# Kernel tuning notes

Hardware: AMD Instinct MI355X
Metric: run time of the kernel (lower is better)

Reference implementation:

```python
import jax, jax.numpy as jnp
import numpy as np

KH = KW = 2  # kernel_size
SH = SW = 2  # stride (== kernel, non-overlapping)

def setup_inputs() -> dict:
    key = jax.random.key(0)
    x = jax.random.normal(key, (64, 256, 112, 112), dtype=jnp.float32)
    return {"x": x}

def reference(x) -> jnp.ndarray:
    # Eval-mode stochastic pool: out = sum_k w_k * (w_k / sum_j w_j) over each
    # KHxKW window of relu(x); windows with zero sum produce 0.
    t = jax.nn.relu(x)
    B, C, H, W = t.shape
    Ho, Wo = H // SH, W // SW
    # stride == kernel -> non-overlapping windows via reshape (matches unfold)
    w = t.reshape(B, C, Ho, KH, Wo, KW).transpose(0, 1, 2, 4, 3, 5)
    w = w.reshape(B, C, Ho, Wo, KH * KW)
    s = w.sum(axis=-1)                      # [B,C,Ho,Wo]
    s_adj = jnp.where(s == 0, jnp.ones_like(s), s)
    out = (w * w).sum(axis=-1) / s_adj      # sum(w * w/sum(w))
    return out
```

## Files before the change

### kernel.cpp

```cpp
#include <hip/hip_runtime.h>


typedef float v4f __attribute__((ext_vector_type(4)));
typedef float v2f __attribute__((ext_vector_type(2)));

#define NCHUNK 28672u
#define CH_IN  7168u
#define CH_OUT 1792u

__global__ __launch_bounds__(256) void stoch_pool2d_kernel(
    const float* __restrict__ in, float* __restrict__ out) {
    __shared__ float lds[CH_IN];
    const unsigned int t = threadIdx.x;

    for (unsigned int c = blockIdx.x; c < NCHUNK; c += gridDim.x) {
        const v4f* src = reinterpret_cast<const v4f*>(in + (size_t)c * CH_IN);

        v4f r[7];
#pragma unroll
        for (int i = 0; i < 7; ++i)
            r[i] = __builtin_nontemporal_load(src + (i * 256u + t));
#pragma unroll
        for (int i = 0; i < 7; ++i)
            reinterpret_cast<v4f*>(lds)[i * 256u + t] = r[i];
        __syncthreads();

        float* dst = out + (size_t)c * CH_OUT;
        const v2f* l2 = reinterpret_cast<const v2f*>(lds);
#pragma unroll
        for (int i = 0; i < 7; ++i) {
            unsigned int o    = i * 256u + t;
            unsigned int orow = o / 56u;
            unsigned int ocol = o - orow * 56u;
            v2f top = l2[(2u * orow)      * 56u + ocol];
            v2f bot = l2[(2u * orow + 1u) * 56u + ocol];

            float a0 = fmaxf(top.x, 0.f), a1 = fmaxf(top.y, 0.f);
            float b0 = fmaxf(bot.x, 0.f), b1 = fmaxf(bot.y, 0.f);
            float s = (a0 + a1) + (b0 + b1);
            float q = (a0 * a0 + a1 * a1) + (b0 * b0 + b1 * b1);
            float v = (s > 0.f) ? q * __builtin_amdgcn_rcpf(s) : 0.f;
            __builtin_nontemporal_store(v, dst + o);
        }
        __syncthreads();
    }
}

extern "C" void kernel_launch(void* const* d_in, const int* in_sizes, int n_in,
                              void* d_out, int out_size, void* d_ws, size_t ws_size,
                              hipStream_t stream) {
    const float* x = (const float*)d_in[0];
    float* out = (float*)d_out;

    const int block = 256;
    const int grid = 2560;
    stoch_pool2d_kernel<<<grid, block, 0, stream>>>(x, out);
}
```

Baseline: 186.7 us.

## Prefetch next chunk into registers and write four outputs per thread

Each block now works through a fixed 14 chunks on a 2048-block grid. It loads the next chunk's input into registers while it computes the current chunk out of LDS, so global loads overlap the LDS pass. The output stage switches from per-element v2f reads and scalar stores to v4f LDS reads and 16-byte vector stores covering four outputs per thread, leaving only 448 of 256x2 threads active. The prefetch doubles register use for the staged data, which can lower occupancy, and the grid size is now hardcoded to match this exact input shape.

```diff
diff --git a/kernel.cpp b/kernel.cpp
--- a/kernel.cpp
+++ b/kernel.cpp
@@ -2,47 +2,77 @@
 
 
 typedef float v4f __attribute__((ext_vector_type(4)));
-typedef float v2f __attribute__((ext_vector_type(2)));
 
 #define NCHUNK 28672u
 #define CH_IN  7168u
 #define CH_OUT 1792u
+#define GRID   2048u
+#define ITERS  14u
+
+__device__ __forceinline__ float pool1(float x0, float x1, float y0, float y1) {
+    float a0 = fmaxf(x0, 0.f), a1 = fmaxf(x1, 0.f);
+    float b0 = fmaxf(y0, 0.f), b1 = fmaxf(y1, 0.f);
+    float s = (a0 + a1) + (b0 + b1);
+    float q = (a0 * a0 + a1 * a1) + (b0 * b0 + b1 * b1);
+    return (s > 0.f) ? q * __builtin_amdgcn_rcpf(s) : 0.f;
+}
 
 __global__ __launch_bounds__(256) void stoch_pool2d_kernel(
     const float* __restrict__ in, float* __restrict__ out) {
     __shared__ float lds[CH_IN];
     const unsigned int t = threadIdx.x;
 
-    for (unsigned int c = blockIdx.x; c < NCHUNK; c += gridDim.x) {
+    unsigned int c = blockIdx.x;
+
+    v4f r[7];
+    {
         const v4f* src = reinterpret_cast<const v4f*>(in + (size_t)c * CH_IN);
-
-        v4f r[7];
 #pragma unroll
         for (int i = 0; i < 7; ++i)
             r[i] = __builtin_nontemporal_load(src + (i * 256u + t));
+    }
+
+    for (unsigned int it = 0; it < ITERS; ++it) {
 #pragma unroll
         for (int i = 0; i < 7; ++i)
             reinterpret_cast<v4f*>(lds)[i * 256u + t] = r[i];
+
+        v4f nxt[7];
+        if (it + 1u < ITERS) {
+            const v4f* src =
+                reinterpret_cast<const v4f*>(in + (size_t)(c + GRID) * CH_IN);
+#pragma unroll
+            for (int i = 0; i < 7; ++i)
+                nxt[i] = __builtin_nontemporal_load(src + (i * 256u + t));
+        }
         __syncthreads();
 
         float* dst = out + (size_t)c * CH_OUT;
-        const v2f* l2 = reinterpret_cast<const v2f*>(lds);
+        const v4f* l4 = reinterpret_cast<const v4f*>(lds);
 #pragma unroll
-        for (int i = 0; i < 7; ++i) {
-            unsigned int o    = i * 256u + t;
-            unsigned int orow = o / 56u;
-            unsigned int ocol = o - orow * 56u;
-            v2f top = l2[(2u * orow)      * 56u + ocol];
-            v2f bot = l2[(2u * orow + 1u) * 56u + ocol];
-
-            float a0 = fmaxf(top.x, 0.f), a1 = fmaxf(top.y, 0.f);
-            float b0 = fmaxf(bot.x, 0.f), b1 = fmaxf(bot.y, 0.f);
-            float s = (a0 + a1) + (b0 + b1);
-            float q = (a0 * a0 + a1 * a1) + (b0 * b0 + b1 * b1);
-            float v = (s > 0.f) ? q * __builtin_amdgcn_rcpf(s) : 0.f;
-            __builtin_nontemporal_store(v, dst + o);
+        for (unsigned int i = 0; i < 2; ++i) {
+            unsigned int o4 = i * 256u + t;
+            if (o4 < 448u) {
+                unsigned int orow = o4 / 14u;
+                unsigned int oc4  = o4 - orow * 14u;
+                unsigned int base = orow * 56u + oc4 * 2u;
+                v4f t0 = l4[base];
+                v4f t1 = l4[base + 1u];
+                v4f b0 = l4[base + 28u];
+                v4f b1 = l4[base + 29u];
+                v4f v;
+                v.x = pool1(t0.x, t0.y, b0.x, b0.y);
+                v.y = pool1(t0.z, t0.w, b0.z, b0.w);
+                v.z = pool1(t1.x, t1.y, b1.x, b1.y);
+                v.w = pool1(t1.z, t1.w, b1.z, b1.w);
+                __builtin_nontemporal_store(v, reinterpret_cast<v4f*>(dst) + o4);
+            }
         }
         __syncthreads();
+
+#pragma unroll
+        for (int i = 0; i < 7; ++i) r[i] = nxt[i];
+        c += GRID;
     }
 }
 
@@ -52,7 +82,5 @@
     const float* x = (const float*)d_in[0];
     float* out = (float*)d_out;
 
-    const int block = 256;
-    const int grid = 2560;
-    stoch_pool2d_kernel<<<grid, block, 0, stream>>>(x, out);
+    stoch_pool2d_kernel<<<GRID, 256, 0, stream>>>(x, out);
 }
```

After: 184.0 us (median of 2 runs). Within noise of the previous version (-1.4%).
